# Kernel tuning notes

Measured on AMD Instinct MI355X. Metric: run time of the kernel, lower is better.

Reference implementation:

```python
import jax, jax.numpy as jnp
import numpy as np

BN_EPS = 1e-3  # keras BatchNormalization default epsilon

@jax.custom_vjp
def ste_sign(x):
    # larq ste_sign: sign(x) with sign(0) -> +1
    return jnp.where(x >= 0, 1.0, -1.0).astype(x.dtype)

def _ste_fwd(x):
    return ste_sign(x), x

def _ste_bwd(x, g):
    # straight-through estimator, gradient clipped to |x| <= 1
    return (g * (jnp.abs(x) <= 1).astype(g.dtype),)

ste_sign.defvjp(_ste_fwd, _ste_bwd)

def setup_inputs() -> dict:
    key = jax.random.key(0)
    k1, k2, k3, k4, k5, k6 = jax.random.split(key, 6)
    B, D_IN, D_H = 32768, 2048, 512
    return {
        "input_tensor": jax.random.normal(k1, (B, D_IN), dtype=jnp.float32),
        "W": jax.random.normal(k2, (D_IN, D_H), dtype=jnp.float32) * 0.05,
        "b": jax.random.normal(k3, (D_H,), dtype=jnp.float32) * 0.01,
        "beta": jax.random.normal(k4, (D_H,), dtype=jnp.float32) * 0.01,
        "moving_mean": jax.random.normal(k5, (D_H,), dtype=jnp.float32) * 0.1,
        "moving_var": jax.random.uniform(k6, (D_H,), dtype=jnp.float32, minval=0.5, maxval=1.5),
    }

def reference(input_tensor, W, b, beta, moving_mean, moving_var):
    # QuantDense: binarize input and kernel, float GEMM over {-1,+1} values
    xq = ste_sign(input_tensor)                # [B, D_in]
    wq = ste_sign(W)                           # [D_in, D_h]
    y = jnp.matmul(xq, wq) + b                 # [B, D_h]
    # BatchNorm inference (training=False), scale=False (no gamma), center=True
    inv = jax.lax.rsqrt(moving_var + BN_EPS)
    return (y - moving_mean) * inv + beta
```

## Files before the change

kernel.cpp:

```cpp
#include <hip/hip_runtime.h>
#include <stdint.h>

#define D_IN 2048
#define D_H  512
#define BM   64
#define NST  16

typedef __attribute__((ext_vector_type(4)))  int i32x4;
typedef __attribute__((ext_vector_type(16))) int i32x16;

__global__ __launch_bounds__(1024) void pack_wt_kernel(
    const float* __restrict__ W, char* __restrict__ Wf) {
  const int s = blockIdx.x;
  const int t = threadIdx.x >> 6;
  const int l = threadIdx.x & 63;
  const int n = t * 32 + (l & 31);
  const int kbase = s * 32 + 16 * (l >> 5);
  uint wq[4];
#pragma unroll
  for (int q = 0; q < 4; ++q) {
    uint w = 0x01010101u;
#pragma unroll
    for (int j = 0; j < 4; ++j) {
      uint bits = __float_as_uint(W[(size_t)(kbase + 4 * q + j) * D_H + n]);
      w ^= ((uint)((int)bits >> 31)) & (0xFEu << (8 * j));
    }
    wq[q] = w;
  }
  *(uint4*)(Wf + ((size_t)(s * 16 + t) * 64 + l) * 16) =
      make_uint4(wq[0], wq[1], wq[2], wq[3]);
}

__device__ __forceinline__ uint pack4(float4 v) {
  uint w = 0x01010101u;
  w ^= ((uint)((int)__float_as_uint(v.x) >> 31)) & 0x000000FEu;
  w ^= ((uint)((int)__float_as_uint(v.y) >> 31)) & 0x0000FE00u;
  w ^= ((uint)((int)__float_as_uint(v.z) >> 31)) & 0x00FE0000u;
  w ^= ((uint)((int)__float_as_uint(v.w) >> 31)) & 0xFE000000u;
  return w;
}

__global__ __launch_bounds__(512) void bgemm_kernel(
    const float* __restrict__ X, const char* __restrict__ Wf,
    const float* __restrict__ b, const float* __restrict__ beta,
    const float* __restrict__ mm, const float* __restrict__ mv,
    float* __restrict__ out) {
  __shared__ __align__(16) char XpL[2][8192];

  const int tid = threadIdx.x;
  const int l   = tid & 63;
  const int wv  = tid >> 6;
  const int am  = l & 31;
  const int ah  = l >> 5;
  const size_t m0 = (size_t)blockIdx.x * BM;
  const int colbase = wv * 64;

  const int r0 = tid >> 5;
  const int kw = tid & 31;
  const float* Xt = X + (m0 + r0) * D_IN + kw * 4;

  const int ws0 = r0 * 128 + (((kw >> 2) ^ (r0 & 7)) << 4) + (kw & 3) * 4;

  const int arow0 = am * 128;
  const int arow1 = arow0 + 32 * 128;
  const int akey  = am & 7;

  const char* Bb0 = Wf + (size_t)(2 * wv) * 1024 + (size_t)l * 16;
  const char* Bb1 = Bb0 + 1024;

  i32x16 acc00, acc01, acc10, acc11;
#pragma unroll
  for (int r = 0; r < 16; ++r) { acc00[r] = 0; acc01[r] = 0; acc10[r] = 0; acc11[r] = 0; }

  float4 vxa, vxb, vxc, vxd;

  vxa = *(const float4*)(Xt);
  vxb = *(const float4*)(Xt + 16 * D_IN);
  vxc = *(const float4*)(Xt + 32 * D_IN);
  vxd = *(const float4*)(Xt + 48 * D_IN);
  *(uint*)(XpL[0] + ws0)        = pack4(vxa);
  *(uint*)(XpL[0] + ws0 + 2048) = pack4(vxb);
  *(uint*)(XpL[0] + ws0 + 4096) = pack4(vxc);
  *(uint*)(XpL[0] + ws0 + 6144) = pack4(vxd);
  __syncthreads();

#pragma unroll 1
  for (int st = 0; st < NST; ++st) {
    const char* buf = &XpL[st & 1][0];
    const size_t so = (size_t)st * 65536;

    i32x4 B0a = *(const i32x4*)(Bb0 + so + 0 * 16384);
    i32x4 B0b = *(const i32x4*)(Bb1 + so + 0 * 16384);
    i32x4 B1a = *(const i32x4*)(Bb0 + so + 1 * 16384);
    i32x4 B1b = *(const i32x4*)(Bb1 + so + 1 * 16384);
    i32x4 B2a = *(const i32x4*)(Bb0 + so + 2 * 16384);
    i32x4 B2b = *(const i32x4*)(Bb1 + so + 2 * 16384);
    i32x4 B3a = *(const i32x4*)(Bb0 + so + 3 * 16384);
    i32x4 B3b = *(const i32x4*)(Bb1 + so + 3 * 16384);

    if (st + 1 < NST) {
      const float* xp = Xt + (st + 1) * 128;
      vxa = *(const float4*)(xp);
      vxb = *(const float4*)(xp + 16 * D_IN);
      vxc = *(const float4*)(xp + 32 * D_IN);
      vxd = *(const float4*)(xp + 48 * D_IN);
    }

    {
      i32x4 a0 = *(const i32x4*)(buf + arow0 + (((0 + ah) ^ akey) << 4));
      i32x4 a1 = *(const i32x4*)(buf + arow1 + (((0 + ah) ^ akey) << 4));
      acc00 = __builtin_amdgcn_mfma_i32_32x32x32_i8(a0, B0a, acc00, 0, 0, 0);
      acc10 = __builtin_amdgcn_mfma_i32_32x32x32_i8(a1, B0a, acc10, 0, 0, 0);
      acc01 = __builtin_amdgcn_mfma_i32_32x32x32_i8(a0, B0b, acc01, 0, 0, 0);
      acc11 = __builtin_amdgcn_mfma_i32_32x32x32_i8(a1, B0b, acc11, 0, 0, 0);
    }
    {
      i32x4 a0 = *(const i32x4*)(buf + arow0 + (((2 + ah) ^ akey) << 4));
      i32x4 a1 = *(const i32x4*)(buf + arow1 + (((2 + ah) ^ akey) << 4));
      acc00 = __builtin_amdgcn_mfma_i32_32x32x32_i8(a0, B1a, acc00, 0, 0, 0);
      acc10 = __builtin_amdgcn_mfma_i32_32x32x32_i8(a1, B1a, acc10, 0, 0, 0);
      acc01 = __builtin_amdgcn_mfma_i32_32x32x32_i8(a0, B1b, acc01, 0, 0, 0);
      acc11 = __builtin_amdgcn_mfma_i32_32x32x32_i8(a1, B1b, acc11, 0, 0, 0);
    }
    {
      i32x4 a0 = *(const i32x4*)(buf + arow0 + (((4 + ah) ^ akey) << 4));
      i32x4 a1 = *(const i32x4*)(buf + arow1 + (((4 + ah) ^ akey) << 4));
      acc00 = __builtin_amdgcn_mfma_i32_32x32x32_i8(a0, B2a, acc00, 0, 0, 0);
      acc10 = __builtin_amdgcn_mfma_i32_32x32x32_i8(a1, B2a, acc10, 0, 0, 0);
      acc01 = __builtin_amdgcn_mfma_i32_32x32x32_i8(a0, B2b, acc01, 0, 0, 0);
      acc11 = __builtin_amdgcn_mfma_i32_32x32x32_i8(a1, B2b, acc11, 0, 0, 0);
    }
    {
      i32x4 a0 = *(const i32x4*)(buf + arow0 + (((6 + ah) ^ akey) << 4));
      i32x4 a1 = *(const i32x4*)(buf + arow1 + (((6 + ah) ^ akey) << 4));
      acc00 = __builtin_amdgcn_mfma_i32_32x32x32_i8(a0, B3a, acc00, 0, 0, 0);
      acc10 = __builtin_amdgcn_mfma_i32_32x32x32_i8(a1, B3a, acc10, 0, 0, 0);
      acc01 = __builtin_amdgcn_mfma_i32_32x32x32_i8(a0, B3b, acc01, 0, 0, 0);
      acc11 = __builtin_amdgcn_mfma_i32_32x32x32_i8(a1, B3b, acc11, 0, 0, 0);
    }

    if (st + 1 < NST) {
      char* nbuf = &XpL[(st + 1) & 1][0];
      *(uint*)(nbuf + ws0)        = pack4(vxa);
      *(uint*)(nbuf + ws0 + 2048) = pack4(vxb);
      *(uint*)(nbuf + ws0 + 4096) = pack4(vxc);
      *(uint*)(nbuf + ws0 + 6144) = pack4(vxd);
    }
    __syncthreads();
  }

  const int rb = 4 * ah;
#pragma unroll
  for (int h = 0; h < 2; ++h) {
#pragma unroll
    for (int nt = 0; nt < 2; ++nt) {
      const i32x16 A = (h == 0) ? ((nt == 0) ? acc00 : acc01)
                                : ((nt == 0) ? acc10 : acc11);
      const int c = colbase + nt * 32 + am;
      const float bb  = b[c];
      const float mmc = mm[c];
      const float bec = beta[c];
      const float inv = rsqrtf(mv[c] + 1e-3f);
#pragma unroll
      for (int r = 0; r < 16; ++r) {
        const int row = (r & 3) + 8 * (r >> 2) + rb + 32 * h;
        out[(m0 + row) * D_H + c] = ((float)A[r] + bb - mmc) * inv + bec;
      }
    }
  }
}

extern "C" void kernel_launch(void* const* d_in, const int* in_sizes, int n_in,
                              void* d_out, int out_size, void* d_ws, size_t ws_size,
                              hipStream_t stream) {
  const float* X    = (const float*)d_in[0];
  const float* W    = (const float*)d_in[1];
  const float* b    = (const float*)d_in[2];
  const float* beta = (const float*)d_in[3];
  const float* mm   = (const float*)d_in[4];
  const float* mv   = (const float*)d_in[5];
  float* out = (float*)d_out;

  char* Wf = (char*)d_ws;

  pack_wt_kernel<<<dim3(D_IN / 32), dim3(1024), 0, stream>>>(W, Wf);

  const int M = in_sizes[0] / D_IN;
  bgemm_kernel<<<dim3(M / BM), dim3(512), 0, stream>>>(X, Wf, b, beta, mm, mv, out);
}
```

Measured before the change: 88.73 us.

## Use 16 waves per block with one 32-column tile per wave and fragment-ordered LDS

Doubles the block to 1024 threads so each wave owns 32 output columns instead of 64, halving per-wave accumulators and B loads. The packed X tile in LDS is laid out directly in MFMA A-fragment order, so each lane reads one contiguous 16-byte chunk instead of using XOR-swizzled row addressing. Each thread now loads two float4 of X per stage instead of four. The goal is more latency hiding and fewer registers per wave, at the cost of heavier barrier synchronization over 16 waves and possible LDS write bank conflicts with the new layout.

After: 98.01 us. 10.5% more time.

```diff
diff --git a/kernel.cpp b/kernel.cpp
--- a/kernel.cpp
+++ b/kernel.cpp
@@ -40,7 +40,7 @@
   return w;
 }
 
-__global__ __launch_bounds__(512) void bgemm_kernel(
+__global__ __launch_bounds__(1024) void bgemm_kernel(
     const float* __restrict__ X, const char* __restrict__ Wf,
     const float* __restrict__ b, const float* __restrict__ beta,
     const float* __restrict__ mm, const float* __restrict__ mv,
@@ -53,119 +53,89 @@
   const int am  = l & 31;
   const int ah  = l >> 5;
   const size_t m0 = (size_t)blockIdx.x * BM;
-  const int colbase = wv * 64;
+  const int cb  = wv * 32;
 
-  const int r0 = tid >> 5;
-  const int kw = tid & 31;
-  const float* Xt = X + (m0 + r0) * D_IN + kw * 4;
+  const int xr = tid >> 4;
+  const int c0 = tid & 15;
+  const float4* X4row = (const float4*)(X + (m0 + xr) * D_IN);
 
-  const int ws0 = r0 * 128 + (((kw >> 2) ^ (r0 & 7)) << 4) + (kw & 3) * 4;
+  const int ws0 = ((xr >> 5) * 4 + (c0 >> 3)) * 1024
+                + ((xr & 31) + 32 * ((c0 >> 2) & 1)) * 16 + 4 * (c0 & 3);
+  const int ws1 = ws0 + 2048;
 
-  const int arow0 = am * 128;
-  const int arow1 = arow0 + 32 * 128;
-  const int akey  = am & 7;
+  const int alane = l * 16;
 
-  const char* Bb0 = Wf + (size_t)(2 * wv) * 1024 + (size_t)l * 16;
-  const char* Bb1 = Bb0 + 1024;
+  const char* Bb = Wf + (size_t)wv * 1024 + (size_t)l * 16;
 
-  i32x16 acc00, acc01, acc10, acc11;
+  i32x16 acc0, acc1;
 #pragma unroll
-  for (int r = 0; r < 16; ++r) { acc00[r] = 0; acc01[r] = 0; acc10[r] = 0; acc11[r] = 0; }
+  for (int r = 0; r < 16; ++r) { acc0[r] = 0; acc1[r] = 0; }
 
-  float4 vxa, vxb, vxc, vxd;
+  float4 vx0, vx1;
 
-  vxa = *(const float4*)(Xt);
-  vxb = *(const float4*)(Xt + 16 * D_IN);
-  vxc = *(const float4*)(Xt + 32 * D_IN);
-  vxd = *(const float4*)(Xt + 48 * D_IN);
-  *(uint*)(XpL[0] + ws0)        = pack4(vxa);
-  *(uint*)(XpL[0] + ws0 + 2048) = pack4(vxb);
-  *(uint*)(XpL[0] + ws0 + 4096) = pack4(vxc);
-  *(uint*)(XpL[0] + ws0 + 6144) = pack4(vxd);
+  vx0 = X4row[c0];
+  vx1 = X4row[c0 + 16];
+  *(uint*)(&XpL[0][0] + ws0) = pack4(vx0);
+  *(uint*)(&XpL[0][0] + ws1) = pack4(vx1);
   __syncthreads();
 
 #pragma unroll 1
   for (int st = 0; st < NST; ++st) {
+    const size_t so = (size_t)st * 65536;
+    i32x4 B0 = *(const i32x4*)(Bb + so);
+    i32x4 B1 = *(const i32x4*)(Bb + so + 16384);
+    i32x4 B2 = *(const i32x4*)(Bb + so + 32768);
+    i32x4 B3 = *(const i32x4*)(Bb + so + 49152);
+    if (st + 1 < NST) {
+      vx0 = X4row[(st + 1) * 32 + c0];
+      vx1 = X4row[(st + 1) * 32 + c0 + 16];
+    }
     const char* buf = &XpL[st & 1][0];
-    const size_t so = (size_t)st * 65536;
-
-    i32x4 B0a = *(const i32x4*)(Bb0 + so + 0 * 16384);
-    i32x4 B0b = *(const i32x4*)(Bb1 + so + 0 * 16384);
-    i32x4 B1a = *(const i32x4*)(Bb0 + so + 1 * 16384);
-    i32x4 B1b = *(const i32x4*)(Bb1 + so + 1 * 16384);
-    i32x4 B2a = *(const i32x4*)(Bb0 + so + 2 * 16384);
-    i32x4 B2b = *(const i32x4*)(Bb1 + so + 2 * 16384);
-    i32x4 B3a = *(const i32x4*)(Bb0 + so + 3 * 16384);
-    i32x4 B3b = *(const i32x4*)(Bb1 + so + 3 * 16384);
-
-    if (st + 1 < NST) {
-      const float* xp = Xt + (st + 1) * 128;
-      vxa = *(const float4*)(xp);
-      vxb = *(const float4*)(xp + 16 * D_IN);
-      vxc = *(const float4*)(xp + 32 * D_IN);
-      vxd = *(const float4*)(xp + 48 * D_IN);
-    }
-
     {
-      i32x4 a0 = *(const i32x4*)(buf + arow0 + (((0 + ah) ^ akey) << 4));
-      i32x4 a1 = *(const i32x4*)(buf + arow1 + (((0 + ah) ^ akey) << 4));
-      acc00 = __builtin_amdgcn_mfma_i32_32x32x32_i8(a0, B0a, acc00, 0, 0, 0);
-      acc10 = __builtin_amdgcn_mfma_i32_32x32x32_i8(a1, B0a, acc10, 0, 0, 0);
-      acc01 = __builtin_amdgcn_mfma_i32_32x32x32_i8(a0, B0b, acc01, 0, 0, 0);
-      acc11 = __builtin_amdgcn_mfma_i32_32x32x32_i8(a1, B0b, acc11, 0, 0, 0);
+      i32x4 a0 = *(const i32x4*)(buf + 0 * 1024 + alane);
+      i32x4 a1 = *(const i32x4*)(buf + 4096 + 0 * 1024 + alane);
+      acc0 = __builtin_amdgcn_mfma_i32_32x32x32_i8(a0, B0, acc0, 0, 0, 0);
+      acc1 = __builtin_amdgcn_mfma_i32_32x32x32_i8(a1, B0, acc1, 0, 0, 0);
     }
     {
-      i32x4 a0 = *(const i32x4*)(buf + arow0 + (((2 + ah) ^ akey) << 4));
-      i32x4 a1 = *(const i32x4*)(buf + arow1 + (((2 + ah) ^ akey) << 4));
-      acc00 = __builtin_amdgcn_mfma_i32_32x32x32_i8(a0, B1a, acc00, 0, 0, 0);
-      acc10 = __builtin_amdgcn_mfma_i32_32x32x32_i8(a1, B1a, acc10, 0, 0, 0);
-      acc01 = __builtin_amdgcn_mfma_i32_32x32x32_i8(a0, B1b, acc01, 0, 0, 0);
-      acc11 = __builtin_amdgcn_mfma_i32_32x32x32_i8(a1, B1b, acc11, 0, 0, 0);
+      i32x4 a0 = *(const i32x4*)(buf + 1 * 1024 + alane);
+      i32x4 a1 = *(const i32x4*)(buf + 4096 + 1 * 1024 + alane);
+      acc0 = __builtin_amdgcn_mfma_i32_32x32x32_i8(a0, B1, acc0, 0, 0, 0);
+      acc1 = __builtin_amdgcn_mfma_i32_32x32x32_i8(a1, B1, acc1, 0, 0, 0);
     }
     {
-      i32x4 a0 = *(const i32x4*)(buf + arow0 + (((4 + ah) ^ akey) << 4));
-      i32x4 a1 = *(const i32x4*)(buf + arow1 + (((4 + ah) ^ akey) << 4));
-      acc00 = __builtin_amdgcn_mfma_i32_32x32x32_i8(a0, B2a, acc00, 0, 0, 0);
-      acc10 = __builtin_amdgcn_mfma_i32_32x32x32_i8(a1, B2a, acc10, 0, 0, 0);
-      acc01 = __builtin_amdgcn_mfma_i32_32x32x32_i8(a0, B2b, acc01, 0, 0, 0);
-      acc11 = __builtin_amdgcn_mfma_i32_32x32x32_i8(a1, B2b, acc11, 0, 0, 0);
+      i32x4 a0 = *(const i32x4*)(buf + 2 * 1024 + alane);
+      i32x4 a1 = *(const i32x4*)(buf + 4096 + 2 * 1024 + alane);
+      acc0 = __builtin_amdgcn_mfma_i32_32x32x32_i8(a0, B2, acc0, 0, 0, 0);
+      acc1 = __builtin_amdgcn_mfma_i32_32x32x32_i8(a1, B2, acc1, 0, 0, 0);
     }
     {
-      i32x4 a0 = *(const i32x4*)(buf + arow0 + (((6 + ah) ^ akey) << 4));
-      i32x4 a1 = *(const i32x4*)(buf + arow1 + (((6 + ah) ^ akey) << 4));
-      acc00 = __builtin_amdgcn_mfma_i32_32x32x32_i8(a0, B3a, acc00, 0, 0, 0);
-      acc10 = __builtin_amdgcn_mfma_i32_32x32x32_i8(a1, B3a, acc10, 0, 0, 0);
-      acc01 = __builtin_amdgcn_mfma_i32_32x32x32_i8(a0, B3b, acc01, 0, 0, 0);
-      acc11 = __builtin_amdgcn_mfma_i32_32x32x32_i8(a1, B3b, acc11, 0, 0, 0);
+      i32x4 a0 = *(const i32x4*)(buf + 3 * 1024 + alane);
+      i32x4 a1 = *(const i32x4*)(buf + 4096 + 3 * 1024 + alane);
+      acc0 = __builtin_amdgcn_mfma_i32_32x32x32_i8(a0, B3, acc0, 0, 0, 0);
+      acc1 = __builtin_amdgcn_mfma_i32_32x32x32_i8(a1, B3, acc1, 0, 0, 0);
     }
-
     if (st + 1 < NST) {
       char* nbuf = &XpL[(st + 1) & 1][0];
-      *(uint*)(nbuf + ws0)        = pack4(vxa);
-      *(uint*)(nbuf + ws0 + 2048) = pack4(vxb);
-      *(uint*)(nbuf + ws0 + 4096) = pack4(vxc);
-      *(uint*)(nbuf + ws0 + 6144) = pack4(vxd);
+      *(uint*)(nbuf + ws0) = pack4(vx0);
+      *(uint*)(nbuf + ws1) = pack4(vx1);
     }
     __syncthreads();
   }
 
   const int rb = 4 * ah;
+  const int c  = cb + am;
+  const float bb  = b[c];
+  const float mmc = mm[c];
+  const float bec = beta[c];
+  const float inv = rsqrtf(mv[c] + 1e-3f);
 #pragma unroll
-  for (int h = 0; h < 2; ++h) {
+  for (int mt = 0; mt < 2; ++mt) {
+    const i32x16 A = (mt == 0) ? acc0 : acc1;
 #pragma unroll
-    for (int nt = 0; nt < 2; ++nt) {
-      const i32x16 A = (h == 0) ? ((nt == 0) ? acc00 : acc01)
-                                : ((nt == 0) ? acc10 : acc11);
-      const int c = colbase + nt * 32 + am;
-      const float bb  = b[c];
-      const float mmc = mm[c];
-      const float bec = beta[c];
-      const float inv = rsqrtf(mv[c] + 1e-3f);
-#pragma unroll
-      for (int r = 0; r < 16; ++r) {
-        const int row = (r & 3) + 8 * (r >> 2) + rb + 32 * h;
-        out[(m0 + row) * D_H + c] = ((float)A[r] + bb - mmc) * inv + bec;
-      }
+    for (int r = 0; r < 16; ++r) {
+      const int row = (r & 3) + 8 * (r >> 2) + rb + 32 * mt;
+      out[(m0 + row) * D_H + c] = ((float)A[r] + bb - mmc) * inv + bec;
     }
   }
 }
@@ -186,5 +156,5 @@
   pack_wt_kernel<<<dim3(D_IN / 32), dim3(1024), 0, stream>>>(W, Wf);
 
   const int M = in_sizes[0] / D_IN;
-  bgemm_kernel<<<dim3(M / BM), dim3(512), 0, stream>>>(X, Wf, b, beta, mm, mv, out);
+  bgemm_kernel<<<dim3(M / BM), dim3(1024), 0, stream>>>(X, Wf, b, beta, mm, mv, out);
 }
```
